# Kernel tuning notes

Hardware: AMD Instinct MI355X
Metric: run time of the kernel (lower is better)

## Reference

```python
import jax, jax.numpy as jnp
import numpy as np

N = 6144      # nodes
DIN = 65      # input_dim (1 time + 64 space coords)
DOUT = 65     # output_dim per head
H = 4         # nheads
EPS = 1e-7
MIN = 1e-15
# curvature c = 1 throughout (MultiHeadGraphAttentionLayer hardcodes curvature=1)

def arcosh(z):
    return jnp.log(z + jnp.sqrt(jnp.maximum(z * z - 1.0, 0.0)))

def hyp_proj(u):
    # project onto hyperboloid: recompute time coord
    y = u[..., 1:]
    t = jnp.sqrt(1.0 + jnp.sum(y * y, -1, keepdims=True))
    return jnp.concatenate([t, y], -1)

def expmap0(u):
    v = u[..., 1:]
    n = jnp.maximum(jnp.linalg.norm(v, axis=-1, keepdims=True), MIN)
    return jnp.concatenate([jnp.cosh(n), jnp.sinh(n) * v / n], -1)

def logmap0(x):
    y = x[..., 1:]
    n = jnp.maximum(jnp.linalg.norm(y, axis=-1, keepdims=True), MIN)
    t = jnp.maximum(x[..., :1], 1.0 + EPS)
    return jnp.concatenate([jnp.zeros_like(t), arcosh(t) * y / n], -1)

def hyp_linear(x, W):
    # HypLinear (use_bias=False, eval mode): mobius_matvec = exp0(log0(x) @ W^T), then proj
    return hyp_proj(expmap0(logmap0(x) @ W.T))

def to_poincare(x):
    return x[..., 1:] / (x[..., :1] + 1.0)

def to_hyperboloid(p):
    s = jnp.sum(p * p, -1, keepdims=True)
    return jnp.concatenate([1.0 + s, 2.0 * p], -1) / jnp.maximum(1.0 - s, MIN)

def mobius_half(v):
    # 0.5 (x) v  (mobius scalar multiplication, c=1)
    n = jnp.maximum(jnp.linalg.norm(v, axis=-1, keepdims=True), MIN)
    return jnp.tanh(0.5 * jnp.arctanh(jnp.minimum(n, 1.0 - EPS))) * v / n

def head(x, adj_t, Wa, Wd, Wo):
    att = hyp_linear(x, Wa)   # [N, DOUT]
    red = hyp_linear(x, Wd)   # [N, DOUT]
    # pairwise hyperboloid sqdist via Minkowski inner product (negate time coord)
    am = att.at[:, 0].multiply(-1.0)
    theta = jnp.maximum(-(am @ att.T), 1.0 + EPS)          # [N, N]
    S = jnp.minimum(arcosh(theta) ** 2, 50.0)
    # coef[i, j] = -adj[j, i] * sqdist for incoming edges (mask = adj^T)
    coef = jnp.where(adj_t > 0.01, -adj_t * S, 0.0)
    # F.normalize along incoming-edge axis (zeros don't change the L2 norm)
    a = coef / jnp.maximum(jnp.linalg.norm(coef, axis=-1, keepdims=True), 1e-12)
    pv = to_poincare(red)                                   # [N, DOUT-1]
    lam = 2.0 / jnp.maximum(1.0 - jnp.sum(pv * pv, -1), MIN)  # conformal factors [N]
    num = (a * lam[None, :]) @ pv                           # [N, DOUT-1]
    den = jnp.sum(jnp.abs(a) * (lam - 1.0)[None, :], -1, keepdims=True)
    m = mobius_half(num / jnp.maximum(den, MIN))            # mobius midpoint
    return hyp_linear(to_hyperboloid(m), Wo)                # [N, DOUT]

def reference(x, adj, W_att, W_data, W_out, W_lin):
    adj_t = adj.T
    hs = jnp.stack([head(x, adj_t, W_att[h], W_data[h], W_out[h]) for h in range(H)], axis=1)  # [N, H, DOUT]
    p = to_poincare(hs).reshape(x.shape[0], -1)             # PoincareBall.concat -> [N, H*(DOUT-1)]
    return hyp_linear(to_hyperboloid(p), W_lin)             # [N, H*DOUT]

def setup_inputs():
    key = jax.random.key(0)
    ks = jax.random.split(key, 8)
    sp = 0.1 * jax.random.normal(ks[0], (N, DIN - 1), jnp.float32)
    x = jnp.concatenate([jnp.sqrt(1.0 + jnp.sum(sp * sp, -1, keepdims=True)), sp], -1)
    adj = (jax.random.uniform(ks[1], (N, N)) < 32.0 / N).astype(jnp.float32)
    adj = jnp.maximum(adj, jnp.eye(N, dtype=jnp.float32))  # every node >=1 incoming edge
    def xavier(k, shape):
        b = (6.0 / (shape[0] + shape[1])) ** 0.5
        return jax.random.uniform(k, shape, jnp.float32, -b, b)
    W_att = jnp.stack([xavier(jax.random.fold_in(ks[2], h), (DOUT, DIN)) for h in range(H)])
    W_data = jnp.stack([xavier(jax.random.fold_in(ks[3], h), (DOUT, DIN)) for h in range(H)])
    W_out = jnp.stack([xavier(jax.random.fold_in(ks[4], h), (DOUT, DOUT)) for h in range(H)])
    W_lin = xavier(ks[5], (H * DOUT, H * (DOUT - 1) + 1))
    return {"x": x, "adj": adj, "W_att": W_att, "W_data": W_data, "W_out": W_out, "W_lin": W_lin}
```

## Files before the change

### kernel.cpp

```cpp
#include <hip/hip_runtime.h>
#include <hip/hip_fp16.h>
#include <math.h>

#define N 6144
#define H 4
#define CAP 128
#define MINF 1e-15f
#define ONE_EPS  1.0000001192092896f
#define ONE_MEPS 0.9999998807907104f

__device__ __forceinline__ float wave_reduce_sum(float v) {
    v += __shfl_xor(v, 32, 64);
    v += __shfl_xor(v, 16, 64);
    v += __shfl_xor(v, 8, 64);
    v += __shfl_xor(v, 4, 64);
    v += __shfl_xor(v, 2, 64);
    v += __shfl_xor(v, 1, 64);
    return v;
}

__device__ __forceinline__ float arcosh_f(float z) {
    return logf(z + sqrtf(fmaxf(z * z - 1.0f, 0.0f)));
}

__device__ __forceinline__ void h8_to_f(float4 r, float* o) {
    __half2* h = (__half2*)&r;
    #pragma unroll
    for (int q = 0; q < 4; q++) {
        float2 f = __half22float2(h[q]);
        o[2 * q + 0] = f.x;
        o[2 * q + 1] = f.y;
    }
}

__device__ __forceinline__ int bitrev4(int t) {
    return ((t & 1) << 3) | ((t & 2) << 1) | ((t & 4) >> 1) | ((t & 8) >> 3);
}

__global__ void k_prep(const float* __restrict__ x, float* __restrict__ lmv,
                       const float* __restrict__ W_att, const float* __restrict__ W_data,
                       const float* __restrict__ W_out, const float* __restrict__ Wl,
                       float* __restrict__ Bp, float* __restrict__ Bo,
                       float* __restrict__ WlT, int* __restrict__ cnt) {
    int b = blockIdx.x;
    if (b < 1536) {
        int i = b * 4 + (threadIdx.x >> 6);
        int lane = threadIdx.x & 63;
        float y = x[i * 65 + 1 + lane];
        float ss = wave_reduce_sum(y * y);
        float n = fmaxf(sqrtf(ss), MINF);
        float t = fmaxf(x[i * 65], ONE_EPS);
        lmv[i * 64 + lane] = arcosh_f(t) * y / n;
    } else if (b < 1728) {
        int tid = (b - 1536) * 256 + threadIdx.x;
        int m = tid >> 12;
        int r = tid & 4095;
        int k = r >> 6, o = r & 63;
        const float* src;
        if (m < 4) src = W_att + m * 65 * 65;
        else if (m < 8) src = W_data + (m - 4) * 65 * 65;
        else src = W_out + (m - 8) * 65 * 65;
        if (m < 8) {
            Bp[m * 4096 + k * 64 + o] = src[(1 + o) * 65 + (1 + k)];
        } else {
            int dk = (k & 3) * 16 + bitrev4(k >> 2);
            Bo[(m - 8) * 4096 + k * 64 + o] = src[(1 + o) * 65 + (1 + dk)];
        }
    } else if (b < 1808) {
        int L = ((b - 1728) * 256 + threadIdx.x) * 4;
        int k = L / 320, o0 = L % 320;
        float v[4];
        #pragma unroll
        for (int q = 0; q < 4; q++) {
            int o = o0 + q;
            v[q] = (o < 259) ? Wl[(size_t)(1 + o) * 257 + 1 + k] : 0.f;
        }
        *(float4*)(WlT + L) = make_float4(v[0], v[1], v[2], v[3]);
    } else {
        cnt[(b - 1808) * 256 + threadIdx.x] = 0;
    }
}

__global__ void __launch_bounds__(256) k_csr_gemm(
        const float* __restrict__ adj, int* __restrict__ cnt, int* __restrict__ idx,
        const float* __restrict__ lmv, const float* __restrict__ Bp,
        __half* __restrict__ kv, float2* __restrict__ a0l) {
    __shared__ float smem[64 * 65];
    if (blockIdx.x < 768) {
        float (*As)[64] = (float(*)[64])smem;
        float (*Bs)[64] = (float(*)[64])(smem + 1024);
        float (*Cs)[65] = (float(*)[65])smem;
        int my = blockIdx.x / 96;
        int ix = blockIdx.x % 96;
        const float* Bb = Bp + (size_t)my * 4096;
        int i0 = ix * 64;
        int tid = threadIdx.x;
        int tx = tid & 15, ty = tid >> 4;
        float acc[4][4] = {};
        for (int k0 = 0; k0 < 64; k0 += 16) {
            {
                int mm = tid >> 2, kq = tid & 3;
                float4 v = *(const float4*)(lmv + (size_t)(i0 + mm) * 64 + k0 + kq * 4);
                As[kq * 4 + 0][mm] = v.x;
                As[kq * 4 + 1][mm] = v.y;
                As[kq * 4 + 2][mm] = v.z;
                As[kq * 4 + 3][mm] = v.w;
            }
            {
                int kk = tid >> 4, o4 = tid & 15;
                float4 bvv = *(const float4*)(Bb + (k0 + kk) * 64 + o4 * 4);
                *(float4*)&Bs[kk][o4 * 4] = bvv;
            }
            __syncthreads();
            #pragma unroll
            for (int kk = 0; kk < 16; kk++) {
                float4 av = *(const float4*)&As[kk][ty * 4];
                float4 bv = *(const float4*)&Bs[kk][tx * 4];
                float a[4] = {av.x, av.y, av.z, av.w};
                float b[4] = {bv.x, bv.y, bv.z, bv.w};
                #pragma unroll
                for (int r = 0; r < 4; r++)
                    #pragma unroll
                    for (int c = 0; c < 4; c++) acc[r][c] += a[r] * b[c];
            }
            __syncthreads();
        }
        #pragma unroll
        for (int r = 0; r < 4; r++)
            #pragma unroll
            for (int c = 0; c < 4; c++)
                Cs[ty * 4 + r][tx * 4 + c] = acc[r][c];
        __syncthreads();
        int w = tid >> 6, lane = tid & 63;
        bool isAtt = my < 4;
        int h = my & 3;
        #pragma unroll 1
        for (int r = 0; r < 16; r++) {
            int row = w * 16 + r;
            int i = i0 + row;
            float u = Cs[row][lane];
            float nn = fmaxf(sqrtf(wave_reduce_sum(u * u)), MINF);
            if (isAtt) {
                float sha = sinhf(nn);
                kv[((size_t)h * N + i) * 128 + lane] = __float2half(sha * u / nn);
                if (lane == 0) a0l[h * N + i].x = coshf(nn);
            } else {
                float shd = sinhf(nn), chd = coshf(nn);
                float pvd = (shd * u / nn) / (chd + 1.0f);
                kv[((size_t)h * N + i) * 128 + 64 + lane] = __float2half(pvd);
                float sp = wave_reduce_sum(pvd * pvd);
                if (lane == 0) a0l[h * N + i].y = 2.0f / fmaxf(1.0f - sp, MINF);
            }
        }
    } else {
        const uint4* a4 = (const uint4*)adj;
        const unsigned STRIDE = 1048576u;
        unsigned e0 = (blockIdx.x - 768) * 256 + threadIdx.x;
        unsigned s0 = 0, s1 = 0, s2 = 0, s3 = 0;
        int ns = 0;
        uint4 v0 = a4[e0];
        uint4 v1 = a4[e0 + STRIDE];
        uint4 v2 = a4[e0 + 2 * STRIDE];
        uint4 v3 = a4[e0 + 3 * STRIDE];
        #pragma unroll
        for (int it = 0; it < 9; it++) {
            uint4 u = (it & 3) == 0 ? v0 : (it & 3) == 1 ? v1
                    : (it & 3) == 2 ? v2 : v3;
            if (it + 4 < 9) {
                uint4 nv = a4[e0 + (unsigned)(it + 4) * STRIDE];
                if ((it & 3) == 0) v0 = nv;
                else if ((it & 3) == 1) v1 = nv;
                else if ((it & 3) == 2) v2 = nv;
                else v3 = nv;
            }
            if (u.x | u.y | u.z | u.w) {
                unsigned uu[4] = {u.x, u.y, u.z, u.w};
                #pragma unroll
                for (int q = 0; q < 4; q++) {
                    if (uu[q]) {
                        unsigned code = (unsigned)(it * 4 + q);
                        if (ns == 0) s0 = code;
                        else if (ns == 1) s1 = code;
                        else if (ns == 2) s2 = code;
                        else if (ns == 3) s3 = code;
                        else {
                            unsigned t = (e0 + (unsigned)it * STRIDE) * 4u + q;
                            int j = t / N;
                            int i = t % N;
                            int pos = atomicAdd(&cnt[i], 1);
                            if (pos < CAP) idx[i * CAP + pos] = j;
                        }
                        ns++;
                    }
                }
            }
        }
        #pragma unroll
        for (int k = 0; k < 4; k++) {
            if (ns > k) {
                unsigned code = (k == 0) ? s0 : (k == 1) ? s1 : (k == 2) ? s2 : s3;
                unsigned it = code >> 2, q = code & 3;
                unsigned t = (e0 + it * STRIDE) * 4u + q;
                int j = t / N;
                int i = t % N;
                int pos = atomicAdd(&cnt[i], 1);
                if (pos < CAP) idx[i * CAP + pos] = j;
            }
        }
    }
}

__global__ void __launch_bounds__(256) k_attn(
        const int* __restrict__ cnt, const int* __restrict__ idx,
        const __half* __restrict__ kv, const float2* __restrict__ a0l,
        float* __restrict__ lm2) {
    int w = threadIdx.x >> 6, lane = threadIdx.x & 63;
    int gb = blockIdx.x;
    int slot = gb & 7;
    int h = slot >> 1;
    int iblk = (gb >> 3) * 2 + (slot & 1);
    int i = iblk * 4 + w;

    const __half* kvh = kv + (size_t)h * N * 128;
    const float2* a0lh = a0l + (size_t)h * N;
    int c = lane & 3, t = lane >> 2;

    float ai[16];
    {
        float4 r0 = *(const float4*)(kvh + (size_t)i * 128 + c * 16);
        float4 r1 = *(const float4*)(kvh + (size_t)i * 128 + c * 16 + 8);
        h8_to_f(r0, ai);
        h8_to_f(r1, ai + 8);
    }
    float ai0 = a0lh[i].x;
    int nn = min(cnt[i], CAP);

    float accd = 0.f, accss = 0.f;
    float accn16[16] = {};
    for (int base = 0; base < nn; base += 16) {
        int tt = base + t;
        bool act = tt < nn;
        int j = act ? idx[i * CAP + tt] : i;
        float2 al = a0lh[j];
        const __half* row = kvh + (size_t)j * 128;
        float4 b0 = *(const float4*)(row + c * 16);
        float4 b1 = *(const float4*)(row + c * 16 + 8);
        float4 p0 = *(const float4*)(row + 64 + c * 16);
        float4 p1 = *(const float4*)(row + 64 + c * 16 + 8);
        float bv[16], pw[16];
        h8_to_f(b0, bv);
        h8_to_f(b1, bv + 8);
        h8_to_f(p0, pw);
        h8_to_f(p1, pw + 8);
        float d = 0.f;
        #pragma unroll
        for (int k = 0; k < 16; k++) d += ai[k] * bv[k];
        d += __shfl_xor(d, 1, 64);
        d += __shfl_xor(d, 2, 64);
        float theta = fmaxf(ai0 * al.x - d, ONE_EPS);
        float ar = arcosh_f(theta);
        float S = fminf(ar * ar, 50.0f);
        if (!act || j == i) S = 0.f;
        float wq = S * al.y;
        if (c == 0) {
            accd += S * (al.y - 1.0f);
            accss += S * S;
        }
        #pragma unroll
        for (int k = 0; k < 16; k++) accn16[k] = fmaf(wq, pw[k], accn16[k]);
    }
    accd = wave_reduce_sum(accd);
    accss = wave_reduce_sum(accss);
    float nrm = fmaxf(sqrtf(accss), 1e-12f);
    float den = fmaxf(accd / nrm, MINF);
    float scl = 1.0f / (nrm * den);

    float r8[8];
    {
        bool b0 = t & 1;
        #pragma unroll
        for (int kk = 0; kk < 8; kk++) {
            float mine = b0 ? accn16[kk + 8] : accn16[kk];
            float send = b0 ? accn16[kk] : accn16[kk + 8];
            r8[kk] = mine + __shfl_xor(send, 4, 64);
        }
    }
    float r4[4];
    {
        bool b1 = t & 2;
        #pragma unroll
        for (int kk = 0; kk < 4; kk++) {
            float mine = b1 ? r8[kk + 4] : r8[kk];
            float send = b1 ? r8[kk] : r8[kk + 4];
            r4[kk] = mine + __shfl_xor(send, 8, 64);
        }
    }
    float r2[2];
    {
        bool b2 = t & 4;
        #pragma unroll
        for (int kk = 0; kk < 2; kk++) {
            float mine = b2 ? r4[kk + 2] : r4[kk];
            float send = b2 ? r4[kk] : r4[kk + 2];
            r2[kk] = mine + __shfl_xor(send, 16, 64);
        }
    }
    float r1;
    {
        bool b3 = t & 8;
        float mine = b3 ? r2[1] : r2[0];
        float send = b3 ? r2[0] : r2[1];
        r1 = mine + __shfl_xor(send, 32, 64);
    }

    float v = -scl * r1;
    float nv = fmaxf(sqrtf(wave_reduce_sum(v * v)), MINF);
    float nc = fminf(nv, ONE_MEPS);
    float mh = tanhf(0.5f * atanhf(nc));
    float md = mh * v / nv;
    float s = wave_reduce_sum(md * md);
    float Dh = fmaxf(1.0f - s, MINF);
    float hb0 = (1.0f + s) / Dh;
    float hbv = 2.0f * md / Dh;
    float nh = fmaxf(2.0f * sqrtf(s) / Dh, MINF);
    float t2 = fmaxf(hb0, ONE_EPS);
    lm2[((size_t)h * N + i) * 64 + lane] = arcosh_f(t2) * hbv / nh;
}

#define PS 272
#define BS5 336
__global__ void __launch_bounds__(256) k_tail(
        const float* __restrict__ lm2, const float* __restrict__ Bo,
        const float* __restrict__ WlT, float* __restrict__ out) {
    __shared__ float smem[5376 + 16 * PS];
    float* As1 = smem;
    float* Bs1 = smem + 1088;
    float* Bs5 = smem;
    float* P   = smem + 5376;

    int i0 = blockIdx.x * 16;
    int tid = threadIdx.x;
    int ty = tid >> 4;
    int tx = tid & 15;

    for (int h = 0; h < H; h++) {
        {
            float4 v = *(const float4*)(lm2 + ((size_t)h * N + i0 + ty) * 64 + tx * 4);
            *(float4*)(As1 + ty * 68 + tx * 4) = v;
        }
        float acc[4] = {0.f, 0.f, 0.f, 0.f};
        for (int k0 = 0; k0 < 64; k0 += 16) {
            {
                *(float4*)(Bs1 + ty * 64 + tx * 4) =
                    *(const float4*)(Bo + (size_t)h * 4096 + (k0 + ty) * 64 + tx * 4);
            }
            __syncthreads();
            #pragma unroll
            for (int kk = 0; kk < 16; kk++) {
                float a = As1[ty * 68 + k0 + kk];
                float4 bv = *(const float4*)(Bs1 + kk * 64 + tx * 4);
                acc[0] += a * bv.x;
                acc[1] += a * bv.y;
                acc[2] += a * bv.z;
                acc[3] += a * bv.w;
            }
            __syncthreads();
        }
        float ss = acc[0] * acc[0] + acc[1] * acc[1] + acc[2] * acc[2] + acc[3] * acc[3];
        ss += __shfl_xor(ss, 1, 64);
        ss += __shfl_xor(ss, 2, 64);
        ss += __shfl_xor(ss, 4, 64);
        ss += __shfl_xor(ss, 8, 64);
        float nn = fmaxf(sqrtf(ss), MINF);
        float sh = sinhf(nn), ch = coshf(nn);
        float* Pr = P + ty * PS + h * 64 + tx * 4;
        Pr[0] = (sh * acc[0] / nn) / (ch + 1.0f);
        Pr[1] = (sh * acc[1] / nn) / (ch + 1.0f);
        Pr[2] = (sh * acc[2] / nn) / (ch + 1.0f);
        Pr[3] = (sh * acc[3] / nn) / (ch + 1.0f);
    }
    __syncthreads();

    {
        float sp = 0.f;
        float4 pl[4];
        #pragma unroll
        for (int q = 0; q < 4; q++) {
            pl[q] = *(const float4*)(P + ty * PS + q * 64 + tx * 4);
            sp += pl[q].x * pl[q].x + pl[q].y * pl[q].y
                + pl[q].z * pl[q].z + pl[q].w * pl[q].w;
        }
        sp += __shfl_xor(sp, 1, 64);
        sp += __shfl_xor(sp, 2, 64);
        sp += __shfl_xor(sp, 4, 64);
        sp += __shfl_xor(sp, 8, 64);
        float Dh = fmaxf(1.0f - sp, MINF);
        float t2 = fmaxf((1.0f + sp) / Dh, ONE_EPS);
        float nh = fmaxf(2.0f * sqrtf(sp) / Dh, MINF);
        float ar2 = arcosh_f(t2);
        #pragma unroll
        for (int q = 0; q < 4; q++) {
            float4 v = pl[q];
            v.x = ar2 * (2.0f * v.x / Dh) / nh;
            v.y = ar2 * (2.0f * v.y / Dh) / nh;
            v.z = ar2 * (2.0f * v.z / Dh) / nh;
            v.w = ar2 * (2.0f * v.w / Dh) / nh;
            *(float4*)(P + ty * PS + q * 64 + tx * 4) = v;
        }
    }
    __syncthreads();

    float acc2[5][4] = {};
    for (int k0 = 0; k0 < 256; k0 += 16) {
        {
            #pragma unroll
            for (int q = 0; q < 5; q++)
                *(float4*)(Bs5 + ty * BS5 + q * 64 + tx * 4) =
                    *(const float4*)(WlT + (size_t)(k0 + ty) * 320 + q * 64 + tx * 4);
        }
        __syncthreads();
        #pragma unroll
        for (int kq = 0; kq < 4; kq++) {
            float4 pv4 = *(const float4*)(P + ty * PS + k0 + kq * 4);
            float av[4] = {pv4.x, pv4.y, pv4.z, pv4.w};
            #pragma unroll
            for (int j = 0; j < 4; j++) {
                float a = av[j];
                int kk = kq * 4 + j;
                #pragma unroll
                for (int q = 0; q < 5; q++) {
                    float4 bv = *(const float4*)(Bs5 + kk * BS5 + q * 64 + tx * 4);
                    acc2[q][0] += a * bv.x;
                    acc2[q][1] += a * bv.y;
                    acc2[q][2] += a * bv.z;
                    acc2[q][3] += a * bv.w;
                }
            }
        }
        __syncthreads();
    }

    float ss2 = 0.f;
    #pragma unroll
    for (int q = 0; q < 5; q++)
        ss2 += acc2[q][0] * acc2[q][0] + acc2[q][1] * acc2[q][1]
             + acc2[q][2] * acc2[q][2] + acc2[q][3] * acc2[q][3];
    ss2 += __shfl_xor(ss2, 1, 64);
    ss2 += __shfl_xor(ss2, 2, 64);
    ss2 += __shfl_xor(ss2, 4, 64);
    ss2 += __shfl_xor(ss2, 8, 64);
    float nv = fmaxf(sqrtf(ss2), MINF);
    float sh2 = sinhf(nv);
    float scale = sh2 / nv;
    size_t ob = (size_t)(i0 + ty) * 260;
    #pragma unroll
    for (int q = 0; q < 4; q++) {
        int o = q * 64 + tx * 4;
        out[ob + 1 + o + 0] = scale * acc2[q][0];
        out[ob + 1 + o + 1] = scale * acc2[q][1];
        out[ob + 1 + o + 2] = scale * acc2[q][2];
        out[ob + 1 + o + 3] = scale * acc2[q][3];
    }
    if (tx == 0) {
        out[ob] = sqrtf(1.0f + sh2 * sh2);
        out[ob + 257] = scale * acc2[4][0];
        out[ob + 258] = scale * acc2[4][1];
        out[ob + 259] = scale * acc2[4][2];
    }
}

extern "C" void kernel_launch(void* const* d_in, const int* in_sizes, int n_in,
                              void* d_out, int out_size, void* d_ws, size_t ws_size,
                              hipStream_t stream) {
    const float* x = (const float*)d_in[0];
    const float* adj = (const float*)d_in[1];
    const float* W_att = (const float*)d_in[2];
    const float* W_data = (const float*)d_in[3];
    const float* W_out = (const float*)d_in[4];
    const float* W_lin = (const float*)d_in[5];
    float* out = (float*)d_out;

    char* ws = (char*)d_ws;
    size_t off = 0;
    auto alloc = [&](size_t bytes) {
        void* ptr = ws + off;
        off += (bytes + 255) & ~(size_t)255;
        return ptr;
    };
    int* cnt = (int*)alloc((size_t)N * 4);
    int* idx = (int*)alloc((size_t)N * CAP * 4);
    float* lmv = (float*)alloc((size_t)N * 64 * 4);
    __half* kv = (__half*)alloc((size_t)H * N * 128 * 2);
    float2* a0l = (float2*)alloc((size_t)H * N * 8);
    float* lm2 = (float*)alloc((size_t)H * N * 64 * 4);
    float* Bp = (float*)alloc((size_t)8 * 4096 * 4);
    float* Bo = (float*)alloc((size_t)4 * 4096 * 4);
    float* WlT = (float*)alloc((size_t)256 * 320 * 4);

    k_prep<<<1832, 256, 0, stream>>>(x, lmv, W_att, W_data, W_out, W_lin,
                                     Bp, Bo, WlT, cnt);
    k_csr_gemm<<<4864, 256, 0, stream>>>(adj, cnt, idx, lmv, Bp, kv, a0l);
    k_attn<<<6144, 256, 0, stream>>>(cnt, idx, kv, a0l, lm2);
    k_tail<<<N / 16, 256, 0, stream>>>(lm2, Bo, WlT, out);
}
```

Before: 309.5 us.

## Split CSR build into 8 segmented counters to reduce atomic contention

The adjacency scan now writes each edge into one of eight per-segment count and index arrays, chosen by block index, so atomics on a node's counter spread across eight addresses. The attention kernel reads all eight segment counts, builds prefix offsets, and maps each edge slot to its segment and position with compare-select logic. k_prep launches more blocks, presumably to zero the larger counter array. This adds index-math overhead per gather, and each segment is capped at 32 entries, which could drop edges if a segment overflows.

```diff
diff --git a/kernel.cpp b/kernel.cpp
--- a/kernel.cpp
+++ b/kernel.cpp
@@ -5,6 +5,7 @@
 #define N 6144
 #define H 4
 #define CAP 128
+#define SCAP 32
 #define MINF 1e-15f
 #define ONE_EPS  1.0000001192092896f
 #define ONE_MEPS 0.9999998807907104f
@@ -156,6 +157,9 @@
         const uint4* a4 = (const uint4*)adj;
         const unsigned STRIDE = 1048576u;
         unsigned e0 = (blockIdx.x - 768) * 256 + threadIdx.x;
+        int seg = blockIdx.x & 7;
+        int* scnt = cnt + seg * N;
+        int* sidx = idx + (size_t)seg * N * SCAP;
         unsigned s0 = 0, s1 = 0, s2 = 0, s3 = 0;
         int ns = 0;
         uint4 v0 = a4[e0];
@@ -187,8 +191,8 @@
                             unsigned t = (e0 + (unsigned)it * STRIDE) * 4u + q;
                             int j = t / N;
                             int i = t % N;
-                            int pos = atomicAdd(&cnt[i], 1);
-                            if (pos < CAP) idx[i * CAP + pos] = j;
+                            int pos = atomicAdd(&scnt[i], 1);
+                            if (pos < SCAP) sidx[i * SCAP + pos] = j;
                         }
                         ns++;
                     }
@@ -203,8 +207,8 @@
                 unsigned t = (e0 + it * STRIDE) * 4u + q;
                 int j = t / N;
                 int i = t % N;
-                int pos = atomicAdd(&cnt[i], 1);
-                if (pos < CAP) idx[i * CAP + pos] = j;
+                int pos = atomicAdd(&scnt[i], 1);
+                if (pos < SCAP) sidx[i * SCAP + pos] = j;
             }
         }
     }
@@ -233,25 +237,43 @@
         h8_to_f(r1, ai + 8);
     }
     float ai0 = a0lh[i].x;
-    int nn = min(cnt[i], CAP);
+
+    int c0 = min(cnt[0 * N + i], SCAP), c1 = min(cnt[1 * N + i], SCAP);
+    int c2 = min(cnt[2 * N + i], SCAP), c3 = min(cnt[3 * N + i], SCAP);
+    int c4 = min(cnt[4 * N + i], SCAP), c5 = min(cnt[5 * N + i], SCAP);
+    int c6 = min(cnt[6 * N + i], SCAP), c7 = min(cnt[7 * N + i], SCAP);
+    int p1 = c0, p2 = p1 + c1, p3 = p2 + c2, p4 = p3 + c3;
+    int p5 = p4 + c4, p6 = p5 + c5, p7 = p6 + c6;
+    int nn = p7 + c7;
 
     float accd = 0.f, accss = 0.f;
     float accn16[16] = {};
     for (int base = 0; base < nn; base += 16) {
         int tt = base + t;
         bool act = tt < nn;
-        int j = act ? idx[i * CAP + tt] : i;
+        int ts = act ? tt : 0;
+        int sg = (ts >= p1) + (ts >= p2) + (ts >= p3) + (ts >= p4)
+               + (ts >= p5) + (ts >= p6) + (ts >= p7);
+        int pc = 0;
+        pc = (ts >= p1) ? p1 : pc;
+        pc = (ts >= p2) ? p2 : pc;
+        pc = (ts >= p3) ? p3 : pc;
+        pc = (ts >= p4) ? p4 : pc;
+        pc = (ts >= p5) ? p5 : pc;
+        pc = (ts >= p6) ? p6 : pc;
+        pc = (ts >= p7) ? p7 : pc;
+        int j = act ? idx[((size_t)sg * N + i) * SCAP + (ts - pc)] : i;
         float2 al = a0lh[j];
         const __half* row = kvh + (size_t)j * 128;
         float4 b0 = *(const float4*)(row + c * 16);
         float4 b1 = *(const float4*)(row + c * 16 + 8);
         float4 p0 = *(const float4*)(row + 64 + c * 16);
-        float4 p1 = *(const float4*)(row + 64 + c * 16 + 8);
+        float4 p1v = *(const float4*)(row + 64 + c * 16 + 8);
         float bv[16], pw[16];
         h8_to_f(b0, bv);
         h8_to_f(b1, bv + 8);
         h8_to_f(p0, pw);
-        h8_to_f(p1, pw + 8);
+        h8_to_f(p1v, pw + 8);
         float d = 0.f;
         #pragma unroll
         for (int k = 0; k < 16; k++) d += ai[k] * bv[k];
@@ -487,8 +509,8 @@
         off += (bytes + 255) & ~(size_t)255;
         return ptr;
     };
-    int* cnt = (int*)alloc((size_t)N * 4);
-    int* idx = (int*)alloc((size_t)N * CAP * 4);
+    int* cnt = (int*)alloc((size_t)8 * N * 4);
+    int* idx = (int*)alloc((size_t)8 * N * SCAP * 4);
     float* lmv = (float*)alloc((size_t)N * 64 * 4);
     __half* kv = (__half*)alloc((size_t)H * N * 128 * 2);
     float2* a0l = (float2*)alloc((size_t)H * N * 8);
@@ -497,7 +519,7 @@
     float* Bo = (float*)alloc((size_t)4 * 4096 * 4);
     float* WlT = (float*)alloc((size_t)256 * 320 * 4);
 
-    k_prep<<<1832, 256, 0, stream>>>(x, lmv, W_att, W_data, W_out, W_lin,
+    k_prep<<<2000, 256, 0, stream>>>(x, lmv, W_att, W_data, W_out, W_lin,
                                      Bp, Bo, WlT, cnt);
     k_csr_gemm<<<4864, 256, 0, stream>>>(adj, cnt, idx, lmv, Bp, kv, a0l);
     k_attn<<<6144, 256, 0, stream>>>(cnt, idx, kv, a0l, lm2);
```

New measurement: 316.5 us. +2.3%, slower.
